# Kernel tuning notes

Measured on AMD Instinct MI355X. Metric: run time of the kernel, lower is better.

The kernel has to match this reference:

```python
import jax, jax.numpy as jnp
import numpy as np

N, E, H, B = 100000, 1600000, 64, 256
EPS = 1e-5


def ln(x, g, b):
    mu = jnp.mean(x, axis=-1, keepdims=True)
    var = jnp.mean((x - mu) ** 2, axis=-1, keepdims=True)
    return (x - mu) * jax.lax.rsqrt(var + EPS) * g + b


def gelu(x):
    # torch nn.GELU default is exact (erf) gelu
    return jax.nn.gelu(x, approximate=False)


def setup_inputs() -> dict:
    key = jax.random.key(0)
    ks = iter(jax.random.split(key, 64))
    nk = lambda: next(ks)
    s = 0.1
    p = {}
    p["x"] = jax.random.normal(nk(), (N, 2), jnp.float32)
    p["edge_attr"] = jax.random.normal(nk(), (E, 2), jnp.float32)
    # node_embed: Linear(2,H) LN GELU Linear(H,H) LN GELU (dropout = eval no-op)
    p["ne_w1"] = jax.random.normal(nk(), (2, H), jnp.float32) * s
    p["ne_b1"] = jnp.zeros((H,), jnp.float32)
    p["ne_g1"] = jnp.ones((H,), jnp.float32)
    p["ne_be1"] = jnp.zeros((H,), jnp.float32)
    p["ne_w2"] = jax.random.normal(nk(), (H, H), jnp.float32) * s
    p["ne_b2"] = jnp.zeros((H,), jnp.float32)
    p["ne_g2"] = jnp.ones((H,), jnp.float32)
    p["ne_be2"] = jnp.zeros((H,), jnp.float32)
    # 3 TrackConv layers: message MLP Linear(H+2,H)+LN, conv output LN, and outer per-layer LN
    p["conv_w"] = jax.random.normal(nk(), (3, H + 2, H), jnp.float32) * s
    p["conv_b"] = jnp.zeros((3, H), jnp.float32)
    p["conv_mg"] = jnp.ones((3, H), jnp.float32)
    p["conv_mb"] = jnp.zeros((3, H), jnp.float32)
    p["conv_ng"] = jnp.ones((3, H), jnp.float32)
    p["conv_nb"] = jnp.zeros((3, H), jnp.float32)
    p["out_ng"] = jnp.ones((3, H), jnp.float32)
    p["out_nb"] = jnp.zeros((3, H), jnp.float32)
    # head MLP: Linear(H,H)+LN+ReLU, Linear(H,H//2)+LN+ReLU, Linear(H//2,1)
    p["m_w1"] = jax.random.normal(nk(), (H, H), jnp.float32) * s
    p["m_b1"] = jnp.zeros((H,), jnp.float32)
    p["m_g1"] = jnp.ones((H,), jnp.float32)
    p["m_be1"] = jnp.zeros((H,), jnp.float32)
    p["m_w2"] = jax.random.normal(nk(), (H, H // 2), jnp.float32) * s
    p["m_b2"] = jnp.zeros((H // 2,), jnp.float32)
    p["m_g2"] = jnp.ones((H // 2,), jnp.float32)
    p["m_be2"] = jnp.zeros((H // 2,), jnp.float32)
    p["m_w3"] = jax.random.normal(nk(), (H // 2, 1), jnp.float32) * s
    p["m_b3"] = jnp.zeros((1,), jnp.float32)
    p["edge_index"] = jax.random.randint(nk(), (2, E), 0, N, dtype=jnp.int32)
    p["batch"] = jnp.sort(jax.random.randint(nk(), (N,), 0, B, dtype=jnp.int32))
    return p


def reference(x, edge_attr,
              ne_w1, ne_b1, ne_g1, ne_be1, ne_w2, ne_b2, ne_g2, ne_be2,
              conv_w, conv_b, conv_mg, conv_mb, conv_ng, conv_nb, out_ng, out_nb,
              m_w1, m_b1, m_g1, m_be1, m_w2, m_b2, m_g2, m_be2, m_w3, m_b3,
              edge_index, batch):
    # node embedding (dropout in eval = identity)
    h = gelu(ln(x @ ne_w1 + ne_b1, ne_g1, ne_be1))
    h = gelu(ln(h @ ne_w2 + ne_b2, ne_g2, ne_be2))
    src, dst = edge_index[0], edge_index[1]  # PyG: message from src (x_j), aggregate at dst
    deg = jax.ops.segment_sum(jnp.ones((E,), h.dtype), dst, num_segments=N)
    deg = jnp.maximum(deg, 1.0)[:, None]
    for l in range(3):
        msg_in = jnp.concatenate([h[src], edge_attr], axis=-1)  # [E, H+2]
        msg = gelu(ln(msg_in @ conv_w[l] + conv_b[l], conv_mg[l], conv_mb[l]))  # [E, H]
        agg = jax.ops.segment_sum(msg, dst, num_segments=N) / deg  # mean aggregate
        conv_out = ln(agg + h, conv_ng[l], conv_nb[l])  # TrackConv: norm(out + residual)
        h = h + ln(conv_out, out_ng[l], out_nb[l])  # outer norm + residual
    # global mean pool over graphs
    cnt = jnp.maximum(jax.ops.segment_sum(jnp.ones((N,), h.dtype), batch, num_segments=B), 1.0)[:, None]
    g = jax.ops.segment_sum(h, batch, num_segments=B) / cnt  # [B, H]
    g = jax.nn.relu(ln(g @ m_w1 + m_b1, m_g1, m_be1))
    g = jax.nn.relu(ln(g @ m_w2 + m_b2, m_g2, m_be2))
    return g @ m_w3 + m_b3  # [B, 1]
```

## Files before the change

### kernel.cpp

```cpp
#include <hip/hip_runtime.h>
#include <math.h>


typedef __attribute__((ext_vector_type(8))) short bfrag;
typedef __attribute__((ext_vector_type(4))) float ffrag;

template <int CTRL>
__device__ __forceinline__ float dpp_mov(float v) {
  return __int_as_float(
      __builtin_amdgcn_update_dpp(0, __float_as_int(v), CTRL, 0xF, 0xF, true));
}

__device__ __forceinline__ float rsum16(float v) {
  v += dpp_mov<0x128>(v);
  v += dpp_mov<0x124>(v);
  v += dpp_mov<0x122>(v);
  v += dpp_mov<0x121>(v);
  return v;
}

__device__ __forceinline__ float wave_sum64(float v) {
  v = rsum16(v);
  v += __shfl_xor(v, 16, 64);
  v += __shfl_xor(v, 32, 64);
  return v;
}

__device__ __forceinline__ float ln_apply(float t, float g, float b) {
  float mu = wave_sum64(t) * 0.015625f;
  float d = t - mu;
  float var = wave_sum64(d * d) * 0.015625f;
  return d * rsqrtf(var + 1e-5f) * g + b;
}

__device__ __forceinline__ float erf_fast(float x) {
  float ax = fabsf(x);
  float p = fmaf(fmaf(fmaf(fmaf(0.078108f, ax, 0.000972f), ax, 0.230389f),
                      ax, 0.278393f), ax, 1.0f);
  p = p * p;
  p = p * p;
  float r = __builtin_amdgcn_rcpf(p);
  return copysignf(1.0f - r, x);
}

__device__ __forceinline__ float gelu_exact(float v) {
  float half = 0.5f * v;
  return fmaf(half, erf_fast(v * 0.70710678118654752440f), half);
}

__device__ __forceinline__ float lane_bcast(float v, int k) {
  return __uint_as_float(__builtin_amdgcn_readlane(__float_as_uint(v), k));
}

__device__ __forceinline__ short f2bf(float f) {
  union { float f; unsigned u; } v; v.f = f;
  unsigned r = v.u + 0x7fffu + ((v.u >> 16) & 1u);
  return (short)(r >> 16);
}

__global__ __launch_bounds__(256) void k_init(
    const float* __restrict__ x,
    const float* __restrict__ w1, const float* __restrict__ b1,
    const float* __restrict__ g1, const float* __restrict__ be1,
    const float* __restrict__ w2, const float* __restrict__ b2,
    const float* __restrict__ g2, const float* __restrict__ be2,
    const float* __restrict__ conv_w, ushort* __restrict__ wt,
    const int* __restrict__ ei, int* __restrict__ csr, float* __restrict__ gz,
    float* __restrict__ h, ushort* __restrict__ hb,
    int n_nodes, int ne, int nzero_g, int oZg, int oHist, int oEmb, int embWaves) {
  const int bid = blockIdx.x;
  const int tid = threadIdx.x;
  if (bid < oZg) {
    const int i = bid * 256 + tid;
    const int k = i % 96, f = (i / 96) % 64, l = i / (96 * 64);
    const float v = (k < 66) ? conv_w[(size_t)l * 66 * 64 + k * 64 + f] : 0.0f;
    wt[i] = (ushort)f2bf(v);
    return;
  }
  if (bid < oHist) {
    const int base = (bid - oZg) * 1024;
    const int lim = min(base + 1024, nzero_g);
    for (int i = base + tid; i < lim; i += 256) gz[i] = 0.0f;
    return;
  }
  if (bid < oEmb) {
    const int i = (bid - oHist) * 256 + tid;
    if (i < ne) atomicAdd(&csr[ei[ne + i]], 1);
    return;
  }
  const int lane = tid & 63;
  const int wid = ((bid - oEmb) * 256 + tid) >> 6;
  const int nw = embWaves;
  float wc[64];
#pragma unroll
  for (int k = 0; k < 64; k++) wc[k] = w2[k * 64 + lane];
  const float w1a = w1[lane], w1b = w1[64 + lane];
  const float vb1 = b1[lane], vg1 = g1[lane], vbe1 = be1[lane];
  const float vb2 = b2[lane], vg2 = g2[lane], vbe2 = be2[lane];
  for (int n = wid; n < n_nodes; n += nw) {
    const float x0 = x[2 * n], x1 = x[2 * n + 1];
    float t = fmaf(x0, w1a, fmaf(x1, w1b, vb1));
    t = gelu_exact(ln_apply(t, vg1, vbe1));
    float a0 = vb2, a1 = 0.f, a2 = 0.f, a3 = 0.f;
#pragma unroll
    for (int k = 0; k < 64; k += 4) {
      a0 = fmaf(lane_bcast(t, k + 0), wc[k + 0], a0);
      a1 = fmaf(lane_bcast(t, k + 1), wc[k + 1], a1);
      a2 = fmaf(lane_bcast(t, k + 2), wc[k + 2], a2);
      a3 = fmaf(lane_bcast(t, k + 3), wc[k + 3], a3);
    }
    float acc = (a0 + a1) + (a2 + a3);
    acc = gelu_exact(ln_apply(acc, vg2, vbe2));
    h[n * 64 + lane] = acc;
    hb[n * 64 + lane] = (ushort)f2bf(acc);
  }
}

__global__ __launch_bounds__(1024) void k_scan_fast(int* __restrict__ buf, int n) {
  __shared__ int wsum[16];
  const int tid = threadIdx.x, lane = tid & 63, w = tid >> 6;
  const int chunk = (((n + 1023) / 1024) + 3) & ~3;
  const int a = min(tid * chunk, n), b = min(a + chunk, n);
  const bool full = (a + chunk <= n);
  int s = 0;
  if (full) {
    const int4* p4 = (const int4*)(buf + a);
#pragma unroll 4
    for (int i = 0; i < chunk / 4; i++) {
      int4 v = p4[i];
      s += v.x + v.y + v.z + v.w;
    }
  } else {
    for (int i = a; i < b; i++) s += buf[i];
  }
  int inc = s;
#pragma unroll
  for (int sh = 1; sh < 64; sh <<= 1) {
    int t = __shfl_up(inc, sh, 64);
    if (lane >= sh) inc += t;
  }
  if (lane == 63) wsum[w] = inc;
  __syncthreads();
  int wb = 0;
  for (int j = 0; j < w; j++) wb += wsum[j];
  int excl = wb + inc - s;
  if (full) {
    int4* p4 = (int4*)(buf + a);
#pragma unroll 4
    for (int i = 0; i < chunk / 4; i++) {
      int4 v = p4[i];
      int4 o;
      o.x = excl; excl += v.x;
      o.y = excl; excl += v.y;
      o.z = excl; excl += v.z;
      o.w = excl; excl += v.w;
      p4[i] = o;
    }
  } else {
    for (int i = a; i < b; i++) { int v = buf[i]; buf[i] = excl; excl += v; }
  }
}

__global__ void k_scatter(const int* __restrict__ ei, const float* __restrict__ ea,
                          int* __restrict__ cursor, int2* __restrict__ edata, int ne) {
  int i = blockIdx.x * blockDim.x + threadIdx.x;
  if (i < ne) {
    const int d = ei[ne + i];
    const int s = ei[i];
    const float2 eav = *(const float2*)(ea + 2 * (size_t)i);
    const unsigned pk = (unsigned)(ushort)f2bf(eav.x) |
                        ((unsigned)(ushort)f2bf(eav.y) << 16);
    const int pos = atomicAdd(&cursor[d], 1);
    edata[pos] = make_int2(s, (int)pk);
  }
}

__global__ __launch_bounds__(256, 3) void k_edge_node(
    const float* __restrict__ h_in, const ushort* __restrict__ hb_in,
    float* __restrict__ h_out, ushort* __restrict__ hb_out,
    const int2* __restrict__ edata, const int* __restrict__ ends,
    const ushort* __restrict__ wt,
    const float* __restrict__ bias, const float* __restrict__ mg,
    const float* __restrict__ mb,
    const float* __restrict__ ng, const float* __restrict__ nb,
    const float* __restrict__ og, const float* __restrict__ ob,
    int n_nodes, int writeHb) {
  __shared__ __align__(16) ushort lwt[64 * 96];
  {
    const uint4* s = (const uint4*)wt;
    uint4* d = (uint4*)lwt;
    for (int i = threadIdx.x; i < 768; i += 256) d[i] = s[i];
  }
  __syncthreads();

  const int lane = threadIdx.x & 63;
  const int grp = lane >> 4, col = lane & 15;
  const int wid = (blockIdx.x * blockDim.x + threadIdx.x) >> 6;
  const int nw = (gridDim.x * blockDim.x) >> 6;

  float vb[4], vg[4], vbb[4];
#pragma unroll
  for (int t = 0; t < 4; t++) {
    const int f = t * 16 + col;
    vb[t] = bias[f]; vg[t] = mg[f]; vbb[t] = mb[f];
  }

  for (int n = wid; n < n_nodes; n += nw) {
    const int start = (n == 0) ? 0 : ends[n - 1];
    const int end = ends[n];
    float aggf[4] = {0.f, 0.f, 0.f, 0.f};

    int p = start;
    int2 ed = edata[p + min(col, end - p - 1)];
    const ushort* hp0 = hb_in + (size_t)ed.x * 64 + grp * 8;
    bfrag A0 = *(const bfrag*)(hp0);
    bfrag A1 = *(const bfrag*)(hp0 + 32);
    int edy = ed.y;

    for (;;) {
      const int rem = min(16, end - p);
      const int pn = p + 16;
      const bool more = pn < end;
      const int nidx = more ? (pn + min(col, end - pn - 1)) : (p + min(col, rem - 1));
      const int2 edn = edata[nidx];

      bfrag A2 = {0, 0, 0, 0, 0, 0, 0, 0};
      if (grp == 0) {
        A2[0] = (short)(edy & 0xffff);
        A2[1] = (short)((unsigned)edy >> 16);
      }

      ffrag acc[4];
#pragma unroll
      for (int t = 0; t < 4; t++) { ffrag c = {vb[t], vb[t], vb[t], vb[t]}; acc[t] = c; }
#pragma unroll
      for (int t = 0; t < 4; t++) {
        const bfrag B = *(const bfrag*)(lwt + (t * 16 + col) * 96 + grp * 8);
        acc[t] = __builtin_amdgcn_mfma_f32_16x16x32_bf16(A0, B, acc[t], 0, 0, 0);
      }
#pragma unroll
      for (int t = 0; t < 4; t++) {
        const bfrag B = *(const bfrag*)(lwt + (t * 16 + col) * 96 + 32 + grp * 8);
        acc[t] = __builtin_amdgcn_mfma_f32_16x16x32_bf16(A1, B, acc[t], 0, 0, 0);
      }
#pragma unroll
      for (int t = 0; t < 4; t++) {
        const bfrag B = *(const bfrag*)(lwt + (t * 16 + col) * 96 + 64 + grp * 8);
        acc[t] = __builtin_amdgcn_mfma_f32_16x16x32_bf16(A2, B, acc[t], 0, 0, 0);
      }

      const ushort* hq = hb_in + (size_t)edn.x * 64 + grp * 8;
      const bfrag N0 = *(const bfrag*)(hq);
      const bfrag N1 = *(const bfrag*)(hq + 32);

      float sx[4], sq[4];
#pragma unroll
      for (int r = 0; r < 4; r++) {
        float s = (acc[0][r] + acc[1][r]) + (acc[2][r] + acc[3][r]);
        float q = fmaf(acc[0][r], acc[0][r], fmaf(acc[1][r], acc[1][r],
                  fmaf(acc[2][r], acc[2][r], acc[3][r] * acc[3][r])));
        sx[r] = s; sq[r] = q;
      }
#pragma unroll
      for (int r = 0; r < 4; r++) sx[r] = rsum16(sx[r]);
#pragma unroll
      for (int r = 0; r < 4; r++) sq[r] = rsum16(sq[r]);
      float iv[4], mi[4], mk[4];
#pragma unroll
      for (int r = 0; r < 4; r++) {
        const float mu = sx[r] * 0.015625f;
        const float var = fmaf(-mu, mu, sq[r] * 0.015625f);
        iv[r] = rsqrtf(var + 1e-5f);
        mi[r] = -mu * iv[r];
        mk[r] = (grp * 4 + r < rem) ? 1.0f : 0.0f;
      }

#pragma unroll
      for (int t = 0; t < 4; t++) {
        float rs = 0.f;
#pragma unroll
        for (int r = 0; r < 4; r++) {
          const float z = fmaf(acc[t][r], iv[r], mi[r]);
          float v = fmaf(z, vg[t], vbb[t]);
          v = gelu_exact(v);
          rs = fmaf(v, mk[r], rs);
        }
        aggf[t] += rs;
      }

      if (!more) break;
      p = pn; A0 = N0; A1 = N1; edy = edn.y;
    }

#pragma unroll
    for (int t = 0; t < 4; t++) {
      float v = aggf[t];
      v += __shfl_xor(v, 16, 64);
      v += __shfl_xor(v, 32, 64);
      aggf[t] = v;
    }

    const float aggl = (grp == 0) ? aggf[0] : (grp == 1) ? aggf[1]
                     : (grp == 2) ? aggf[2] : aggf[3];

    const float dg = fmaxf((float)(end - start), 1.0f);
    const float hv = h_in[(size_t)n * 64 + lane];
    const float a = aggl / dg + hv;
    const float c = ln_apply(a, ng[lane], nb[lane]);
    const float o = ln_apply(c, og[lane], ob[lane]);
    const float outv = hv + o;
    h_out[(size_t)n * 64 + lane] = outv;
    if (writeHb) hb_out[(size_t)n * 64 + lane] = (ushort)f2bf(outv);
  }
}

__global__ void k_pool_seg(const float* __restrict__ h, const int* __restrict__ batch,
                           float* __restrict__ g, float* __restrict__ cnt,
                           int n_nodes, int chunk) {
  const int lane = threadIdx.x & 63;
  const int wid = (blockIdx.x * blockDim.x + threadIdx.x) >> 6;
  const int n0 = wid * chunk;
  if (n0 >= n_nodes) return;
  const int n1 = min(n0 + chunk, n_nodes);
  int cur = batch[n0], c = 0;
  float acc = 0.f;
  for (int n = n0; n < n1; n++) {
    const int b = batch[n];
    if (b != cur) {
      atomicAdd(&g[(size_t)cur * 64 + lane], acc);
      if (lane == 0) atomicAdd(&cnt[cur], (float)c);
      acc = 0.f; c = 0; cur = b;
    }
    acc += h[(size_t)n * 64 + lane];
    c++;
  }
  atomicAdd(&g[(size_t)cur * 64 + lane], acc);
  if (lane == 0) atomicAdd(&cnt[cur], (float)c);
}

__global__ void k_head(const float* __restrict__ g, const float* __restrict__ cnt,
                       const float* __restrict__ w1, const float* __restrict__ b1,
                       const float* __restrict__ g1, const float* __restrict__ be1,
                       const float* __restrict__ w2, const float* __restrict__ b2,
                       const float* __restrict__ g2, const float* __restrict__ be2,
                       const float* __restrict__ w3, const float* __restrict__ b3,
                       float* __restrict__ out, int nb_) {
  const int lane = threadIdx.x & 63;
  const int row = (blockIdx.x * blockDim.x + threadIdx.x) >> 6;
  if (row >= nb_) return;
  const float c = fmaxf(cnt[row], 1.0f);
  const float gv = g[row * 64 + lane] / c;
  float a0 = b1[lane], a1 = 0.f, a2 = 0.f, a3 = 0.f;
#pragma unroll
  for (int k = 0; k < 64; k += 4) {
    a0 = fmaf(lane_bcast(gv, k + 0), w1[(k + 0) * 64 + lane], a0);
    a1 = fmaf(lane_bcast(gv, k + 1), w1[(k + 1) * 64 + lane], a1);
    a2 = fmaf(lane_bcast(gv, k + 2), w1[(k + 2) * 64 + lane], a2);
    a3 = fmaf(lane_bcast(gv, k + 3), w1[(k + 3) * 64 + lane], a3);
  }
  float t = (a0 + a1) + (a2 + a3);
  t = fmaxf(ln_apply(t, g1[lane], be1[lane]), 0.0f);

  const int j = lane & 31;
  float c0 = b2[j], c1 = 0.f, c2 = 0.f, c3 = 0.f;
#pragma unroll
  for (int k = 0; k < 64; k += 4) {
    c0 = fmaf(lane_bcast(t, k + 0), w2[(k + 0) * 32 + j], c0);
    c1 = fmaf(lane_bcast(t, k + 1), w2[(k + 1) * 32 + j], c1);
    c2 = fmaf(lane_bcast(t, k + 2), w2[(k + 2) * 32 + j], c2);
    c3 = fmaf(lane_bcast(t, k + 3), w2[(k + 3) * 32 + j], c3);
  }
  float t2 = (c0 + c1) + (c2 + c3);
  t2 = fmaxf(ln_apply(t2, g2[j], be2[j]), 0.0f);
  const float p = t2 * w3[j];
  const float s = wave_sum64(p) * 0.5f;
  if (lane == 0) out[row] = s + b3[0];
}

extern "C" void kernel_launch(void* const* d_in, const int* in_sizes, int n_in,
                              void* d_out, int out_size, void* d_ws, size_t ws_size,
                              hipStream_t stream) {
  const float* x      = (const float*)d_in[0];
  const float* ea     = (const float*)d_in[1];
  const float* ne_w1  = (const float*)d_in[2];
  const float* ne_b1  = (const float*)d_in[3];
  const float* ne_g1  = (const float*)d_in[4];
  const float* ne_be1 = (const float*)d_in[5];
  const float* ne_w2  = (const float*)d_in[6];
  const float* ne_b2  = (const float*)d_in[7];
  const float* ne_g2  = (const float*)d_in[8];
  const float* ne_be2 = (const float*)d_in[9];
  const float* conv_w = (const float*)d_in[10];
  const float* conv_b = (const float*)d_in[11];
  const float* conv_mg= (const float*)d_in[12];
  const float* conv_mb= (const float*)d_in[13];
  const float* conv_ng= (const float*)d_in[14];
  const float* conv_nb= (const float*)d_in[15];
  const float* out_ng = (const float*)d_in[16];
  const float* out_nb = (const float*)d_in[17];
  const float* m_w1   = (const float*)d_in[18];
  const float* m_b1   = (const float*)d_in[19];
  const float* m_g1   = (const float*)d_in[20];
  const float* m_be1  = (const float*)d_in[21];
  const float* m_w2   = (const float*)d_in[22];
  const float* m_b2   = (const float*)d_in[23];
  const float* m_g2   = (const float*)d_in[24];
  const float* m_be2  = (const float*)d_in[25];
  const float* m_w3   = (const float*)d_in[26];
  const float* m_b3   = (const float*)d_in[27];
  const int*   eidx   = (const int*)d_in[28];
  const int*   batch  = (const int*)d_in[29];
  float* outp = (float*)d_out;

  const int NN = in_sizes[29];
  const int NE = in_sizes[1] / 2;
  const int NB = out_size;

  float* ws = (float*)d_ws;
  float*  h0   = ws;
  float*  h1   = h0 + (size_t)NN * 64;
  float*  gbuf = h1 + (size_t)NN * 64;
  float*  cnt  = gbuf + (size_t)NB * 64;
  ushort* wt   = (ushort*)(cnt + NB);
  ushort* hb0  = wt + 3 * 64 * 96;
  ushort* hb1  = hb0 + (size_t)NN * 64;
  int*    csr  = (int*)(hb1 + (size_t)NN * 64);
  int2*   edata= (int2*)(csr + NN);

  const dim3 blk(256);

  hipMemsetAsync(csr, 0, sizeof(int) * (size_t)NN, stream);

  const int nPrep = (3 * 64 * 96) / 256;
  const int nZg   = (NB * 64 + NB + 1023) / 1024;
  const int nHist = (NE + 255) / 256;
  const int oZg = nPrep, oHist = nPrep + nZg, oEmb = nPrep + nZg + nHist;
  const int embBlocks = 2048;
  k_init<<<oEmb + embBlocks, blk, 0, stream>>>(
      x, ne_w1, ne_b1, ne_g1, ne_be1, ne_w2, ne_b2, ne_g2, ne_be2,
      conv_w, wt, eidx, csr, gbuf, h0, hb0, NN, NE, NB * 64 + NB,
      oZg, oHist, oEmb, embBlocks * 4);

  k_scan_fast<<<1, 1024, 0, stream>>>(csr, NN);
  k_scatter<<<(NE + 255) / 256, blk, 0, stream>>>(eidx, ea, csr, edata, NE);

  float* hin = h0;  float* hout = h1;
  ushort* hbin = hb0; ushort* hbout = hb1;
  for (int l = 0; l < 3; l++) {
    k_edge_node<<<4096, blk, 0, stream>>>(
        hin, hbin, hout, hbout, edata, csr, wt + (size_t)l * 64 * 96,
        conv_b + l * 64, conv_mg + l * 64, conv_mb + l * 64,
        conv_ng + l * 64, conv_nb + l * 64,
        out_ng + l * 64, out_nb + l * 64, NN, (l < 2) ? 1 : 0);
    float* tf = hin; hin = hout; hout = tf;
    ushort* tb = hbin; hbin = hbout; hbout = tb;
  }

  {
    const int chunk = 32;
    const int nwaves = (NN + chunk - 1) / chunk;
    const int nblocks = (nwaves * 64 + 255) / 256;
    k_pool_seg<<<nblocks, blk, 0, stream>>>(hin, batch, gbuf, cnt, NN, chunk);
  }
  k_head<<<(NB + 3) / 4, blk, 0, stream>>>(gbuf, cnt, m_w1, m_b1, m_g1, m_be1,
                                           m_w2, m_b2, m_g2, m_be2, m_w3, m_b3,
                                           outp, NB);
}
```

Before: 829.2 us.

## Fuse global pooling into head via binary-searched segments; simplify GELU arithmetic

Replaces the atomic-based pooling kernel and the separate head kernel with one kernel. Each wave binary-searches the sorted batch array to find its graph's node range, sums those rows directly and then runs the head MLP. This drops the pool-buffer zeroing, the float atomics and one launch. The catch is that it relies on batch being sorted, and only 256 waves each read about 390 rows serially. It also rewrites the GELU approximation with fewer operations (a select instead of copysign plus fma).

```diff
diff --git a/kernel.cpp b/kernel.cpp
--- a/kernel.cpp
+++ b/kernel.cpp
@@ -33,19 +33,16 @@
   return d * rsqrtf(var + 1e-5f) * g + b;
 }
 
-__device__ __forceinline__ float erf_fast(float x) {
-  float ax = fabsf(x);
+__device__ __forceinline__ float gelu_fast(float v) {
+  float ax = fabsf(v) * 0.70710678118654752440f;
   float p = fmaf(fmaf(fmaf(fmaf(0.078108f, ax, 0.000972f), ax, 0.230389f),
                       ax, 0.278393f), ax, 1.0f);
   p = p * p;
   p = p * p;
   float r = __builtin_amdgcn_rcpf(p);
-  return copysignf(1.0f - r, x);
-}
-
-__device__ __forceinline__ float gelu_exact(float v) {
-  float half = 0.5f * v;
-  return fmaf(half, erf_fast(v * 0.70710678118654752440f), half);
+  float hr = 0.5f * r;
+  float sel = (v >= 0.0f) ? (1.0f - hr) : hr;
+  return v * sel;
 }
 
 __device__ __forceinline__ float lane_bcast(float v, int k) {
@@ -65,22 +62,16 @@
     const float* __restrict__ w2, const float* __restrict__ b2,
     const float* __restrict__ g2, const float* __restrict__ be2,
     const float* __restrict__ conv_w, ushort* __restrict__ wt,
-    const int* __restrict__ ei, int* __restrict__ csr, float* __restrict__ gz,
+    const int* __restrict__ ei, int* __restrict__ csr,
     float* __restrict__ h, ushort* __restrict__ hb,
-    int n_nodes, int ne, int nzero_g, int oZg, int oHist, int oEmb, int embWaves) {
+    int n_nodes, int ne, int oHist, int oEmb, int embWaves) {
   const int bid = blockIdx.x;
   const int tid = threadIdx.x;
-  if (bid < oZg) {
+  if (bid < oHist) {
     const int i = bid * 256 + tid;
     const int k = i % 96, f = (i / 96) % 64, l = i / (96 * 64);
     const float v = (k < 66) ? conv_w[(size_t)l * 66 * 64 + k * 64 + f] : 0.0f;
     wt[i] = (ushort)f2bf(v);
-    return;
-  }
-  if (bid < oHist) {
-    const int base = (bid - oZg) * 1024;
-    const int lim = min(base + 1024, nzero_g);
-    for (int i = base + tid; i < lim; i += 256) gz[i] = 0.0f;
     return;
   }
   if (bid < oEmb) {
@@ -100,7 +91,7 @@
   for (int n = wid; n < n_nodes; n += nw) {
     const float x0 = x[2 * n], x1 = x[2 * n + 1];
     float t = fmaf(x0, w1a, fmaf(x1, w1b, vb1));
-    t = gelu_exact(ln_apply(t, vg1, vbe1));
+    t = gelu_fast(ln_apply(t, vg1, vbe1));
     float a0 = vb2, a1 = 0.f, a2 = 0.f, a3 = 0.f;
 #pragma unroll
     for (int k = 0; k < 64; k += 4) {
@@ -110,7 +101,7 @@
       a3 = fmaf(lane_bcast(t, k + 3), wc[k + 3], a3);
     }
     float acc = (a0 + a1) + (a2 + a3);
-    acc = gelu_exact(ln_apply(acc, vg2, vbe2));
+    acc = gelu_fast(ln_apply(acc, vg2, vbe2));
     h[n * 64 + lane] = acc;
     hb[n * 64 + lane] = (ushort)f2bf(acc);
   }
@@ -282,7 +273,7 @@
         for (int r = 0; r < 4; r++) {
           const float z = fmaf(acc[t][r], iv[r], mi[r]);
           float v = fmaf(z, vg[t], vbb[t]);
-          v = gelu_exact(v);
+          v = gelu_fast(v);
           rs = fmaf(v, mk[r], rs);
         }
         aggf[t] += rs;
@@ -314,63 +305,58 @@
   }
 }
 
-__global__ void k_pool_seg(const float* __restrict__ h, const int* __restrict__ batch,
-                           float* __restrict__ g, float* __restrict__ cnt,
-                           int n_nodes, int chunk) {
-  const int lane = threadIdx.x & 63;
-  const int wid = (blockIdx.x * blockDim.x + threadIdx.x) >> 6;
-  const int n0 = wid * chunk;
-  if (n0 >= n_nodes) return;
-  const int n1 = min(n0 + chunk, n_nodes);
-  int cur = batch[n0], c = 0;
-  float acc = 0.f;
-  for (int n = n0; n < n1; n++) {
-    const int b = batch[n];
-    if (b != cur) {
-      atomicAdd(&g[(size_t)cur * 64 + lane], acc);
-      if (lane == 0) atomicAdd(&cnt[cur], (float)c);
-      acc = 0.f; c = 0; cur = b;
-    }
-    acc += h[(size_t)n * 64 + lane];
-    c++;
-  }
-  atomicAdd(&g[(size_t)cur * 64 + lane], acc);
-  if (lane == 0) atomicAdd(&cnt[cur], (float)c);
-}
-
-__global__ void k_head(const float* __restrict__ g, const float* __restrict__ cnt,
-                       const float* __restrict__ w1, const float* __restrict__ b1,
-                       const float* __restrict__ g1, const float* __restrict__ be1,
-                       const float* __restrict__ w2, const float* __restrict__ b2,
-                       const float* __restrict__ g2, const float* __restrict__ be2,
-                       const float* __restrict__ w3, const float* __restrict__ b3,
-                       float* __restrict__ out, int nb_) {
+__global__ __launch_bounds__(256) void k_pool_head(
+    const float* __restrict__ h, const int* __restrict__ batch,
+    const float* __restrict__ w1, const float* __restrict__ b1,
+    const float* __restrict__ g1, const float* __restrict__ be1,
+    const float* __restrict__ w2, const float* __restrict__ b2,
+    const float* __restrict__ g2, const float* __restrict__ be2,
+    const float* __restrict__ w3, const float* __restrict__ b3,
+    float* __restrict__ out, int n_nodes, int nb_) {
   const int lane = threadIdx.x & 63;
   const int row = (blockIdx.x * blockDim.x + threadIdx.x) >> 6;
   if (row >= nb_) return;
-  const float c = fmaxf(cnt[row], 1.0f);
-  const float gv = g[row * 64 + lane] / c;
-  float a0 = b1[lane], a1 = 0.f, a2 = 0.f, a3 = 0.f;
+
+  int lo = 0, hi = n_nodes;
+  while (lo < hi) { int mid = (lo + hi) >> 1; if (batch[mid] < row) lo = mid + 1; else hi = mid; }
+  const int start = lo;
+  hi = n_nodes;
+  while (lo < hi) { int mid = (lo + hi) >> 1; if (batch[mid] <= row) lo = mid + 1; else hi = mid; }
+  const int end = lo;
+
+  float a0 = 0.f, a1 = 0.f, a2 = 0.f, a3 = 0.f;
+  int n = start;
+  for (; n + 4 <= end; n += 4) {
+    a0 += h[(size_t)(n + 0) * 64 + lane];
+    a1 += h[(size_t)(n + 1) * 64 + lane];
+    a2 += h[(size_t)(n + 2) * 64 + lane];
+    a3 += h[(size_t)(n + 3) * 64 + lane];
+  }
+  for (; n < end; n++) a0 += h[(size_t)n * 64 + lane];
+  const float cgt = fmaxf((float)(end - start), 1.0f);
+  const float gv = ((a0 + a1) + (a2 + a3)) / cgt;
+
+  float c0 = b1[lane], c1 = 0.f, c2 = 0.f, c3 = 0.f;
 #pragma unroll
   for (int k = 0; k < 64; k += 4) {
-    a0 = fmaf(lane_bcast(gv, k + 0), w1[(k + 0) * 64 + lane], a0);
-    a1 = fmaf(lane_bcast(gv, k + 1), w1[(k + 1) * 64 + lane], a1);
-    a2 = fmaf(lane_bcast(gv, k + 2), w1[(k + 2) * 64 + lane], a2);
-    a3 = fmaf(lane_bcast(gv, k + 3), w1[(k + 3) * 64 + lane], a3);
-  }
-  float t = (a0 + a1) + (a2 + a3);
+    c0 = fmaf(lane_bcast(gv, k + 0), w1[(k + 0) * 64 + lane], c0);
+    c1 = fmaf(lane_bcast(gv, k + 1), w1[(k + 1) * 64 + lane], c1);
+    c2 = fmaf(lane_bcast(gv, k + 2), w1[(k + 2) * 64 + lane], c2);
+    c3 = fmaf(lane_bcast(gv, k + 3), w1[(k + 3) * 64 + lane], c3);
+  }
+  float t = (c0 + c1) + (c2 + c3);
   t = fmaxf(ln_apply(t, g1[lane], be1[lane]), 0.0f);
 
   const int j = lane & 31;
-  float c0 = b2[j], c1 = 0.f, c2 = 0.f, c3 = 0.f;
+  float d0 = b2[j], d1 = 0.f, d2 = 0.f, d3 = 0.f;
 #pragma unroll
   for (int k = 0; k < 64; k += 4) {
-    c0 = fmaf(lane_bcast(t, k + 0), w2[(k + 0) * 32 + j], c0);
-    c1 = fmaf(lane_bcast(t, k + 1), w2[(k + 1) * 32 + j], c1);
-    c2 = fmaf(lane_bcast(t, k + 2), w2[(k + 2) * 32 + j], c2);
-    c3 = fmaf(lane_bcast(t, k + 3), w2[(k + 3) * 32 + j], c3);
-  }
-  float t2 = (c0 + c1) + (c2 + c3);
+    d0 = fmaf(lane_bcast(t, k + 0), w2[(k + 0) * 32 + j], d0);
+    d1 = fmaf(lane_bcast(t, k + 1), w2[(k + 1) * 32 + j], d1);
+    d2 = fmaf(lane_bcast(t, k + 2), w2[(k + 2) * 32 + j], d2);
+    d3 = fmaf(lane_bcast(t, k + 3), w2[(k + 3) * 32 + j], d3);
+  }
+  float t2 = (d0 + d1) + (d2 + d3);
   t2 = fmaxf(ln_apply(t2, g2[j], be2[j]), 0.0f);
   const float p = t2 * w3[j];
   const float s = wave_sum64(p) * 0.5f;
@@ -419,9 +405,7 @@
   float* ws = (float*)d_ws;
   float*  h0   = ws;
   float*  h1   = h0 + (size_t)NN * 64;
-  float*  gbuf = h1 + (size_t)NN * 64;
-  float*  cnt  = gbuf + (size_t)NB * 64;
-  ushort* wt   = (ushort*)(cnt + NB);
+  ushort* wt   = (ushort*)(h1 + (size_t)NN * 64);
   ushort* hb0  = wt + 3 * 64 * 96;
   ushort* hb1  = hb0 + (size_t)NN * 64;
   int*    csr  = (int*)(hb1 + (size_t)NN * 64);
@@ -432,14 +416,12 @@
   hipMemsetAsync(csr, 0, sizeof(int) * (size_t)NN, stream);
 
   const int nPrep = (3 * 64 * 96) / 256;
-  const int nZg   = (NB * 64 + NB + 1023) / 1024;
   const int nHist = (NE + 255) / 256;
-  const int oZg = nPrep, oHist = nPrep + nZg, oEmb = nPrep + nZg + nHist;
+  const int oHist = nPrep, oEmb = nPrep + nHist;
   const int embBlocks = 2048;
   k_init<<<oEmb + embBlocks, blk, 0, stream>>>(
       x, ne_w1, ne_b1, ne_g1, ne_be1, ne_w2, ne_b2, ne_g2, ne_be2,
-      conv_w, wt, eidx, csr, gbuf, h0, hb0, NN, NE, NB * 64 + NB,
-      oZg, oHist, oEmb, embBlocks * 4);
+      conv_w, wt, eidx, csr, h0, hb0, NN, NE, oHist, oEmb, embBlocks * 4);
 
   k_scan_fast<<<1, 1024, 0, stream>>>(csr, NN);
   k_scatter<<<(NE + 255) / 256, blk, 0, stream>>>(eidx, ea, csr, edata, NE);
@@ -456,13 +438,7 @@
     ushort* tb = hbin; hbin = hbout; hbout = tb;
   }
 
-  {
-    const int chunk = 32;
-    const int nwaves = (NN + chunk - 1) / chunk;
-    const int nblocks = (nwaves * 64 + 255) / 256;
-    k_pool_seg<<<nblocks, blk, 0, stream>>>(hin, batch, gbuf, cnt, NN, chunk);
-  }
-  k_head<<<(NB + 3) / 4, blk, 0, stream>>>(gbuf, cnt, m_w1, m_b1, m_g1, m_be1,
-                                           m_w2, m_b2, m_g2, m_be2, m_w3, m_b3,
-                                           outp, NB);
-}
+  k_pool_head<<<(NB + 3) / 4, blk, 0, stream>>>(
+      hin, batch, m_w1, m_b1, m_g1, m_be1, m_w2, m_b2, m_g2, m_be2,
+      m_w3, m_b3, outp, NN, NB);
+}
```

Measured after the change: 873.3 us. +5.3%, slower.
